# Performance work log

Hardware: AMD Instinct MI355X
Metric: run time of the kernel (lower is better)

Reference implementation:

```python
import jax, jax.numpy as jnp
import numpy as np

B, F, V, E = 16384, 20, 100000, 32
D_BOT = F * E            # 640
DIMS = (512, 256)        # bottom MLP dims
TDIMS = (128, 64)        # tower hidden dims
N_DOM = 4


def setup_inputs() -> dict:
    key = jax.random.key(0)
    ks = jax.random.split(key, 16)
    inp = {
        "feature_ids": jax.random.randint(ks[0], (B, F), 0, V, dtype=jnp.int64),
        "domain_id": jax.random.randint(ks[1], (B,), 0, N_DOM, dtype=jnp.int64),
        # embedding tables [F, V, E]
        "emb": jax.random.normal(ks[2], (F, V, E), dtype=jnp.float32) * 0.01,
        # bottom MLP: 640 -> 512 -> 256 (relu, no output layer)
        "W1": jax.random.normal(ks[3], (D_BOT, DIMS[0]), dtype=jnp.float32) * (1.0 / np.sqrt(D_BOT)),
        "b1": jnp.zeros((DIMS[0],), dtype=jnp.float32),
        "W2": jax.random.normal(ks[4], (DIMS[0], DIMS[1]), dtype=jnp.float32) * (1.0 / np.sqrt(DIMS[0])),
        "b2": jnp.zeros((DIMS[1],), dtype=jnp.float32),
        # towers (stacked over domain dim): 256 -> 128 -> 64 -> 1
        "TW1": jax.random.normal(ks[5], (N_DOM, DIMS[1], TDIMS[0]), dtype=jnp.float32) * (1.0 / np.sqrt(DIMS[1])),
        "Tb1": jnp.zeros((N_DOM, TDIMS[0]), dtype=jnp.float32),
        "TW2": jax.random.normal(ks[6], (N_DOM, TDIMS[0], TDIMS[1]), dtype=jnp.float32) * (1.0 / np.sqrt(TDIMS[0])),
        "Tb2": jnp.zeros((N_DOM, TDIMS[1]), dtype=jnp.float32),
        "TW3": jax.random.normal(ks[7], (N_DOM, TDIMS[1], 1), dtype=jnp.float32) * (1.0 / np.sqrt(TDIMS[1])),
        "Tb3": jnp.zeros((N_DOM, 1), dtype=jnp.float32),
    }
    return inp


def reference(feature_ids, domain_id, emb, W1, b1, W2, b2, TW1, Tb1, TW2, Tb2, TW3, Tb3):
    # Embedding lookup + concat: [B, F, E] -> [B, F*E]
    e = emb[jnp.arange(F)[None, :], feature_ids]          # [B, F, E]
    h = e.reshape(B, F * E)
    # Shared bottom MLP (relu)
    h = jax.nn.relu(h @ W1 + b1)                          # [B, 512]
    h = jax.nn.relu(h @ W2 + b2)                          # [B, 256]
    # All domain towers computed densely for every sample (faithful to source)
    t = jax.nn.relu(jnp.einsum('bi,dio->bdo', h, TW1) + Tb1[None])   # [B, D, 128]
    t = jax.nn.relu(jnp.einsum('bdi,dio->bdo', t, TW2) + Tb2[None])  # [B, D, 64]
    logit = jnp.einsum('bdi,dio->bdo', t, TW3) + Tb3[None]           # [B, D, 1]
    ys = jax.nn.sigmoid(logit)[..., 0]                    # [B, D]
    # Select per-sample domain output via mask (domains are exclusive)
    onehot = jax.nn.one_hot(domain_id, N_DOM, dtype=ys.dtype)        # [B, D]
    final = jnp.sum(ys * onehot, axis=1)                  # [B]
    return final
```

## Files before the change

### kernel.cpp

```cpp
#include <hip/hip_runtime.h>

#define B_SZ  16384
#define F_SZ  20
#define V_SZ  100000
#define E_SZ  32
#define DBOT  640
#define D1    512
#define D2    256
#define T1D   128
#define T2D   64
#define NDOM  4

typedef __bf16 bf16x8 __attribute__((ext_vector_type(8)));
typedef float  f32x4  __attribute__((ext_vector_type(4)));

#define MFMA(a, b, c) __builtin_amdgcn_mfma_f32_16x16x32_bf16((a), (b), (c), 0, 0, 0)

__global__ __launch_bounds__(256) void k_prep(const float* __restrict__ W1,
                                              const float* __restrict__ W2,
                                              const float* __restrict__ TW1,
                                              const float* __restrict__ TW2,
                                              __bf16* __restrict__ W1P,
                                              __bf16* __restrict__ W2P,
                                              __bf16* __restrict__ TW1P,
                                              __bf16* __restrict__ TW2P,
                                              int* __restrict__ cnt) {
  int bid = blockIdx.x, tid = threadIdx.x;
  const float* src; __bf16* dst; int n, k, N;
  if (bid < 160) {
    long g = (long)bid * 256 + tid;
    int lane = g & 63; int kkg = (int)((g >> 6) % 20); int ntile = (int)(g / 1280);
    n = ntile * 16 + (lane & 15); k = kkg * 32 + ((lane >> 4) << 3);
    src = W1; N = D1; dst = W1P + g * 8;
  } else if (bid < 224) {
    long g = (long)(bid - 160) * 256 + tid;
    int lane = g & 63; int kkg = (int)((g >> 6) & 15); int ntile = (int)(g >> 10);
    n = ntile * 16 + (lane & 15); k = kkg * 32 + ((lane >> 4) << 3);
    src = W2; N = D2; dst = W2P + g * 8;
  } else if (bid < 288) {
    long g = (long)(bid - 224) * 256 + tid;
    int d = (int)(g >> 12); long r = g & 4095;
    int lane = r & 63; int kkg = (int)((r >> 6) & 7); int ntile = (int)(r >> 9);
    n = ntile * 16 + (lane & 15); k = kkg * 32 + ((lane >> 4) << 3);
    src = TW1 + (long)d * D2 * T1D; N = T1D;
    dst = TW1P + ((long)(d * 64 + ntile * 8 + kkg) * 64 + lane) * 8;
  } else if (bid < 304) {
    long g = (long)(bid - 288) * 256 + tid;
    int d = (int)(g >> 10); long r = g & 1023;
    int lane = r & 63; int kkg = (int)((r >> 6) & 3); int ntile = (int)(r >> 8);
    n = ntile * 16 + (lane & 15); k = kkg * 32 + ((lane >> 4) << 3);
    src = TW2 + (long)d * T1D * T2D; N = T2D;
    dst = TW2P + ((long)(d * 16 + ntile * 4 + kkg) * 64 + lane) * 8;
  } else {
    if (tid < NDOM) cnt[tid] = 0;
    return;
  }
  bf16x8 o;
#pragma unroll
  for (int e = 0; e < 8; ++e) o[e] = (__bf16)src[(long)(k + e) * N + n];
  *(bf16x8*)dst = o;
}

__global__ __launch_bounds__(512) void k_fused(const int* __restrict__ fids,
                                               const int* __restrict__ dom,
                                               const float* __restrict__ emb,
                                               const __bf16* __restrict__ W1P,
                                               const float* __restrict__ b1,
                                               const __bf16* __restrict__ W2P,
                                               const float* __restrict__ b2,
                                               __bf16* __restrict__ h2,
                                               int* __restrict__ cnt,
                                               int* __restrict__ lists) {
  __shared__ int    ids_lds[64 * F_SZ];
  __shared__ __bf16 sA[64 * DBOT];
  __shared__ __bf16 h1[64 * D1];

  int bid = blockIdx.x, tid = threadIdx.x;
  int lane = tid & 63, w = tid >> 6;
  int lrow = lane & 15, kq = lane >> 4;
  int m0 = bid * 64;

  if (bid < 64 && tid < 256) {
    int i = bid * 256 + tid;
    int d = dom[i];
    int pl = tid & 63;
#pragma unroll
    for (int dd = 0; dd < NDOM; ++dd) {
      unsigned long long md = __ballot(d == dd);
      if (d == dd) {
        int myoff = __popcll(md & ((1ull << pl) - 1ull));
        int leader = __ffsll((long long)md) - 1;
        int base = 0;
        if (pl == leader) base = atomicAdd(&cnt[dd], __popcll(md));
        base = __shfl(base, leader);
        lists[dd * B_SZ + base + myoff] = i;
      }
    }
  }

  for (int i = tid; i < 64 * F_SZ; i += 512) ids_lds[i] = fids[m0 * F_SZ + i];
  __syncthreads();

  float4 ga[10], gb[10];
  int sb[10];
  {
#pragma unroll
    for (int i = 0; i < 10; ++i) {
      unsigned c = tid + i * 512;
      unsigned row = c / 80;
      unsigned cc = c - row * 80;
      int f = cc >> 2, es = (cc & 3) << 3;
      int id = ids_lds[row * F_SZ + f];
      const float* p = emb + ((long)f * V_SZ + id) * E_SZ + es;
      ga[i] = *(const float4*)p;
      gb[i] = *(const float4*)(p + 4);
      sb[i] = (int)(row * 1280 + cc * 16) ^ ((row & 7) << 4);
    }
#pragma unroll
    for (int i = 0; i < 10; ++i) {
      bf16x8 o;
      o[0] = (__bf16)ga[i].x; o[1] = (__bf16)ga[i].y;
      o[2] = (__bf16)ga[i].z; o[3] = (__bf16)ga[i].w;
      o[4] = (__bf16)gb[i].x; o[5] = (__bf16)gb[i].y;
      o[6] = (__bf16)gb[i].z; o[7] = (__bf16)gb[i].w;
      *(bf16x8*)((char*)sA + sb[i]) = o;
    }
  }
  __syncthreads();

  f32x4 acc[4][4] = {};
#pragma unroll
  for (int f = 0; f < F_SZ; ++f) {
    bf16x8 af[4];
#pragma unroll
    for (int mi = 0; mi < 4; ++mi) {
      int byte = ((mi * 16 + lrow) * 1280 + (f * 32 + kq * 8) * 2) ^ ((lrow & 7) << 4);
      af[mi] = *(const bf16x8*)((const char*)sA + byte);
    }
#pragma unroll
    for (int ni = 0; ni < 4; ++ni) {
      bf16x8 bfr = *(const bf16x8*)(W1P +
          ((long)((w * 4 + ni) * 20 + f) * 64 + lane) * 8);
#pragma unroll
      for (int mi = 0; mi < 4; ++mi)
        acc[mi][ni] = MFMA(af[mi], bfr, acc[mi][ni]);
    }
  }

#pragma unroll
  for (int ni = 0; ni < 4; ++ni) {
    int col = w * 64 + ni * 16 + lrow;
    float bv = b1[col];
#pragma unroll
    for (int mi = 0; mi < 4; ++mi) {
#pragma unroll
      for (int r = 0; r < 4; ++r) {
        int row = mi * 16 + kq * 4 + r;
        float v = acc[mi][ni][r] + bv;
        v = v > 0.f ? v : 0.f;
        int byte = (row * 1024 + col * 2) ^ ((row & 7) << 4);
        *(__bf16*)((char*)h1 + byte) = (__bf16)v;
      }
    }
  }
  __syncthreads();

  f32x4 acc2[4][2] = {};
#pragma unroll 4
  for (int kkg = 0; kkg < 16; ++kkg) {
    bf16x8 a2[4];
#pragma unroll
    for (int mi = 0; mi < 4; ++mi) {
      int byte = ((mi * 16 + lrow) * 1024 + kkg * 64 + kq * 16) ^ ((lrow & 7) << 4);
      a2[mi] = *(const bf16x8*)((const char*)h1 + byte);
    }
#pragma unroll
    for (int ni = 0; ni < 2; ++ni) {
      bf16x8 bfr = *(const bf16x8*)(W2P +
          ((long)((w * 2 + ni) * 16 + kkg) * 64 + lane) * 8);
#pragma unroll
      for (int mi = 0; mi < 4; ++mi)
        acc2[mi][ni] = MFMA(a2[mi], bfr, acc2[mi][ni]);
    }
  }

#pragma unroll
  for (int ni = 0; ni < 2; ++ni) {
    int col = w * 32 + ni * 16 + lrow;
    float bv = b2[col];
#pragma unroll
    for (int mi = 0; mi < 4; ++mi) {
#pragma unroll
      for (int r = 0; r < 4; ++r) {
        long row = m0 + mi * 16 + kq * 4 + r;
        float v = acc2[mi][ni][r] + bv;
        v = v > 0.f ? v : 0.f;
        h2[row * D2 + col] = (__bf16)v;
      }
    }
  }
}

__global__ __launch_bounds__(256) void k_tower(const __bf16* __restrict__ h2,
                                               const __bf16* __restrict__ TW1P,
                                               const __bf16* __restrict__ TW2P,
                                               const float* __restrict__ Tb1,
                                               const float* __restrict__ Tb2,
                                               const float* __restrict__ TW3,
                                               const float* __restrict__ Tb3,
                                               const int* __restrict__ cnt,
                                               const int* __restrict__ lists,
                                               float* __restrict__ out) {
  __shared__ __bf16 t_lds[4][16 * 128];
  int d  = blockIdx.y;
  int nc = cnt[d];
  int base = blockIdx.x * 64;
  if (base >= nc) return;

  int tid  = threadIdx.x;
  int lane = tid & 63;
  int w    = tid >> 6;
  int row  = lane & 15;
  int kq   = lane >> 4;
  int slot = base + w * 16 + row;
  bool valid = slot < nc;
  int m0r = lists[d * B_SZ + (valid ? slot : 0)];

  bf16x8 a1[8];
#pragma unroll
  for (int kk = 0; kk < 8; ++kk)
    a1[kk] = *(const bf16x8*)(h2 + (long)m0r * D2 + kk * 32 + kq * 8);

  f32x4 acc1[8] = {};
#pragma unroll
  for (int kk = 0; kk < 8; ++kk) {
#pragma unroll
    for (int ni = 0; ni < 8; ++ni) {
      bf16x8 b = *(const bf16x8*)(TW1P +
          ((long)(d * 64 + ni * 8 + kk) * 64 + lane) * 8);
      acc1[ni] = MFMA(a1[kk], b, acc1[ni]);
    }
  }
#pragma unroll
  for (int ni = 0; ni < 8; ++ni) {
    float bv = Tb1[d * T1D + ni * 16 + row];
#pragma unroll
    for (int r = 0; r < 4; ++r) {
      float v = acc1[ni][r] + bv;
      v = v > 0.f ? v : 0.f;
      t_lds[w][(kq * 4 + r) * 128 + ni * 16 + row] = (__bf16)v;
    }
  }
  asm volatile("s_waitcnt lgkmcnt(0)" ::: "memory");

  bf16x8 a2[4];
#pragma unroll
  for (int kk = 0; kk < 4; ++kk)
    a2[kk] = *(const bf16x8*)(&t_lds[w][row * 128 + kk * 32 + kq * 8]);
  f32x4 acc2[4] = {};
#pragma unroll
  for (int kk = 0; kk < 4; ++kk) {
#pragma unroll
    for (int ni = 0; ni < 4; ++ni) {
      bf16x8 b = *(const bf16x8*)(TW2P +
          ((long)(d * 16 + ni * 4 + kk) * 64 + lane) * 8);
      acc2[ni] = MFMA(a2[kk], b, acc2[ni]);
    }
  }
  asm volatile("s_waitcnt lgkmcnt(0)" ::: "memory");
#pragma unroll
  for (int ni = 0; ni < 4; ++ni) {
    float bv = Tb2[d * T2D + ni * 16 + row];
#pragma unroll
    for (int r = 0; r < 4; ++r) {
      float v = acc2[ni][r] + bv;
      v = v > 0.f ? v : 0.f;
      t_lds[w][(kq * 4 + r) * 64 + ni * 16 + row] = (__bf16)v;
    }
  }
  asm volatile("s_waitcnt lgkmcnt(0)" ::: "memory");

  float s = 0.f;
#pragma unroll
  for (int j = 0; j < 16; ++j)
    s += (float)t_lds[w][row * 64 + kq * 16 + j] * TW3[d * T2D + kq * 16 + j];
  s += __shfl_xor(s, 16);
  s += __shfl_xor(s, 32);
  s += Tb3[d];
  if (valid && kq == 0)
    out[m0r] = 1.0f / (1.0f + expf(-s));
}

extern "C" void kernel_launch(void* const* d_in, const int* in_sizes, int n_in,
                              void* d_out, int out_size, void* d_ws, size_t ws_size,
                              hipStream_t stream) {
  const int*   fids = (const int*)d_in[0];
  const int*   dom  = (const int*)d_in[1];
  const float* emb  = (const float*)d_in[2];
  const float* W1   = (const float*)d_in[3];
  const float* b1   = (const float*)d_in[4];
  const float* W2   = (const float*)d_in[5];
  const float* b2   = (const float*)d_in[6];
  const float* TW1  = (const float*)d_in[7];
  const float* Tb1  = (const float*)d_in[8];
  const float* TW2  = (const float*)d_in[9];
  const float* Tb2  = (const float*)d_in[10];
  const float* TW3  = (const float*)d_in[11];
  const float* Tb3  = (const float*)d_in[12];
  float* out = (float*)d_out;

  char* ws = (char*)d_ws;
  __bf16* W1P   = (__bf16*)(ws);
  __bf16* W2P   = (__bf16*)(ws + 655360);
  __bf16* TW1P  = (__bf16*)(ws + 917504);
  __bf16* TW2P  = (__bf16*)(ws + 1179648);
  __bf16* h2    = (__bf16*)(ws + 1245184);
  int*    lists = (int*)(ws + 9633792);
  int*    cnt   = (int*)(ws + 9895936);

  k_prep<<<305, 256, 0, stream>>>(W1, W2, TW1, TW2, W1P, W2P, TW1P, TW2P, cnt);
  k_fused<<<256, 512, 0, stream>>>(fids, dom, emb, W1P, b1, W2P, b2, h2,
                                   cnt, lists);
  k_tower<<<dim3(80, NDOM), 256, 0, stream>>>(h2, TW1P, TW2P, Tb1, Tb2,
                                              TW3, Tb3, cnt, lists, out);
}
```

Baseline: 53.16 us.

## Fuse tower MLPs into bottom-MLP kernel, computing all domains densely per tile

Merges the tower stage into the bottom-MLP kernel so h2 stays in LDS rather than going through global memory, and drops the separate tower launch. The per-domain bucketing with atomics and lists is replaced by computing all four towers densely for each 64-row tile and writing only the matching domain's output. This removes a kernel launch, the global h2 round trip and the atomic compaction, at the cost of four times the tower FLOPs and a larger shared-memory footprint (about 149 KB) that limits occupancy.

Result: faster. 50.03 us (-5.9%).

```diff
diff --git a/kernel.cpp b/kernel.cpp
--- a/kernel.cpp
+++ b/kernel.cpp
@@ -23,8 +23,7 @@
                                               __bf16* __restrict__ W1P,
                                               __bf16* __restrict__ W2P,
                                               __bf16* __restrict__ TW1P,
-                                              __bf16* __restrict__ TW2P,
-                                              int* __restrict__ cnt) {
+                                              __bf16* __restrict__ TW2P) {
   int bid = blockIdx.x, tid = threadIdx.x;
   const float* src; __bf16* dst; int n, k, N;
   if (bid < 160) {
@@ -44,16 +43,13 @@
     n = ntile * 16 + (lane & 15); k = kkg * 32 + ((lane >> 4) << 3);
     src = TW1 + (long)d * D2 * T1D; N = T1D;
     dst = TW1P + ((long)(d * 64 + ntile * 8 + kkg) * 64 + lane) * 8;
-  } else if (bid < 304) {
+  } else {
     long g = (long)(bid - 288) * 256 + tid;
     int d = (int)(g >> 10); long r = g & 1023;
     int lane = r & 63; int kkg = (int)((r >> 6) & 3); int ntile = (int)(r >> 8);
     n = ntile * 16 + (lane & 15); k = kkg * 32 + ((lane >> 4) << 3);
     src = TW2 + (long)d * T1D * T2D; N = T2D;
     dst = TW2P + ((long)(d * 16 + ntile * 4 + kkg) * 64 + lane) * 8;
-  } else {
-    if (tid < NDOM) cnt[tid] = 0;
-    return;
   }
   bf16x8 o;
 #pragma unroll
@@ -61,49 +57,38 @@
   *(bf16x8*)dst = o;
 }
 
-__global__ __launch_bounds__(512) void k_fused(const int* __restrict__ fids,
-                                               const int* __restrict__ dom,
-                                               const float* __restrict__ emb,
-                                               const __bf16* __restrict__ W1P,
-                                               const float* __restrict__ b1,
-                                               const __bf16* __restrict__ W2P,
-                                               const float* __restrict__ b2,
-                                               __bf16* __restrict__ h2,
-                                               int* __restrict__ cnt,
-                                               int* __restrict__ lists) {
-  __shared__ int    ids_lds[64 * F_SZ];
-  __shared__ __bf16 sA[64 * DBOT];
-  __shared__ __bf16 h1[64 * D1];
+__global__ __launch_bounds__(512) void k_mega(const int* __restrict__ fids,
+                                              const int* __restrict__ dom,
+                                              const float* __restrict__ emb,
+                                              const __bf16* __restrict__ W1P,
+                                              const float* __restrict__ b1,
+                                              const __bf16* __restrict__ W2P,
+                                              const float* __restrict__ b2,
+                                              const __bf16* __restrict__ TW1P,
+                                              const __bf16* __restrict__ TW2P,
+                                              const float* __restrict__ Tb1,
+                                              const float* __restrict__ Tb2,
+                                              const float* __restrict__ TW3,
+                                              const float* __restrict__ Tb3,
+                                              float* __restrict__ out) {
+  __shared__ __attribute__((aligned(16))) char smem[152576];
+  int*    ids_lds = (int*)(smem + 147456);
+  __bf16* sA      = (__bf16*)smem;
+  __bf16* h1      = (__bf16*)(smem + 81920);
+  __bf16* h2_lds  = (__bf16*)smem;
+  __bf16* t_lds   = (__bf16*)(smem + 32768);
 
   int bid = blockIdx.x, tid = threadIdx.x;
   int lane = tid & 63, w = tid >> 6;
   int lrow = lane & 15, kq = lane >> 4;
   int m0 = bid * 64;
 
-  if (bid < 64 && tid < 256) {
-    int i = bid * 256 + tid;
-    int d = dom[i];
-    int pl = tid & 63;
-#pragma unroll
-    for (int dd = 0; dd < NDOM; ++dd) {
-      unsigned long long md = __ballot(d == dd);
-      if (d == dd) {
-        int myoff = __popcll(md & ((1ull << pl) - 1ull));
-        int leader = __ffsll((long long)md) - 1;
-        int base = 0;
-        if (pl == leader) base = atomicAdd(&cnt[dd], __popcll(md));
-        base = __shfl(base, leader);
-        lists[dd * B_SZ + base + myoff] = i;
-      }
-    }
-  }
-
   for (int i = tid; i < 64 * F_SZ; i += 512) ids_lds[i] = fids[m0 * F_SZ + i];
   __syncthreads();
 
-  float4 ga[10], gb[10];
-  int sb[10];
-  {
+  {
+    float4 ga[10], gb[10];
+    int sb[10];
 #pragma unroll
     for (int i = 0; i < 10; ++i) {
       unsigned c = tid + i * 512;
@@ -128,167 +113,160 @@
   }
   __syncthreads();
 
-  f32x4 acc[4][4] = {};
-#pragma unroll
-  for (int f = 0; f < F_SZ; ++f) {
-    bf16x8 af[4];
-#pragma unroll
-    for (int mi = 0; mi < 4; ++mi) {
-      int byte = ((mi * 16 + lrow) * 1280 + (f * 32 + kq * 8) * 2) ^ ((lrow & 7) << 4);
-      af[mi] = *(const bf16x8*)((const char*)sA + byte);
+  {
+    f32x4 acc[4][4] = {};
+#pragma unroll
+    for (int f = 0; f < F_SZ; ++f) {
+      bf16x8 af[4];
+#pragma unroll
+      for (int mi = 0; mi < 4; ++mi) {
+        int byte = ((mi * 16 + lrow) * 1280 + (f * 32 + kq * 8) * 2) ^ ((lrow & 7) << 4);
+        af[mi] = *(const bf16x8*)((const char*)sA + byte);
+      }
+#pragma unroll
+      for (int ni = 0; ni < 4; ++ni) {
+        bf16x8 bfr = *(const bf16x8*)(W1P +
+            ((long)((w * 4 + ni) * 20 + f) * 64 + lane) * 8);
+#pragma unroll
+        for (int mi = 0; mi < 4; ++mi)
+          acc[mi][ni] = MFMA(af[mi], bfr, acc[mi][ni]);
+      }
     }
 #pragma unroll
     for (int ni = 0; ni < 4; ++ni) {
-      bf16x8 bfr = *(const bf16x8*)(W1P +
-          ((long)((w * 4 + ni) * 20 + f) * 64 + lane) * 8);
-#pragma unroll
-      for (int mi = 0; mi < 4; ++mi)
-        acc[mi][ni] = MFMA(af[mi], bfr, acc[mi][ni]);
-    }
-  }
-
-#pragma unroll
-  for (int ni = 0; ni < 4; ++ni) {
-    int col = w * 64 + ni * 16 + lrow;
-    float bv = b1[col];
-#pragma unroll
-    for (int mi = 0; mi < 4; ++mi) {
-#pragma unroll
-      for (int r = 0; r < 4; ++r) {
-        int row = mi * 16 + kq * 4 + r;
-        float v = acc[mi][ni][r] + bv;
-        v = v > 0.f ? v : 0.f;
-        int byte = (row * 1024 + col * 2) ^ ((row & 7) << 4);
-        *(__bf16*)((char*)h1 + byte) = (__bf16)v;
-      }
-    }
-  }
-  __syncthreads();
-
-  f32x4 acc2[4][2] = {};
+      int col = w * 64 + ni * 16 + lrow;
+      float bv = b1[col];
+#pragma unroll
+      for (int mi = 0; mi < 4; ++mi) {
+#pragma unroll
+        for (int r = 0; r < 4; ++r) {
+          int row = mi * 16 + kq * 4 + r;
+          float v = acc[mi][ni][r] + bv;
+          v = v > 0.f ? v : 0.f;
+          int byte = (row * 1024 + col * 2) ^ ((row & 7) << 4);
+          *(__bf16*)((char*)h1 + byte) = (__bf16)v;
+        }
+      }
+    }
+  }
+  __syncthreads();
+
+  {
+    f32x4 acc2[4][2] = {};
 #pragma unroll 4
-  for (int kkg = 0; kkg < 16; ++kkg) {
-    bf16x8 a2[4];
-#pragma unroll
-    for (int mi = 0; mi < 4; ++mi) {
-      int byte = ((mi * 16 + lrow) * 1024 + kkg * 64 + kq * 16) ^ ((lrow & 7) << 4);
-      a2[mi] = *(const bf16x8*)((const char*)h1 + byte);
+    for (int kkg = 0; kkg < 16; ++kkg) {
+      bf16x8 a2[4];
+#pragma unroll
+      for (int mi = 0; mi < 4; ++mi) {
+        int byte = ((mi * 16 + lrow) * 1024 + kkg * 64 + kq * 16) ^ ((lrow & 7) << 4);
+        a2[mi] = *(const bf16x8*)((const char*)h1 + byte);
+      }
+#pragma unroll
+      for (int ni = 0; ni < 2; ++ni) {
+        bf16x8 bfr = *(const bf16x8*)(W2P +
+            ((long)((w * 2 + ni) * 16 + kkg) * 64 + lane) * 8);
+#pragma unroll
+        for (int mi = 0; mi < 4; ++mi)
+          acc2[mi][ni] = MFMA(a2[mi], bfr, acc2[mi][ni]);
+      }
     }
 #pragma unroll
     for (int ni = 0; ni < 2; ++ni) {
-      bf16x8 bfr = *(const bf16x8*)(W2P +
-          ((long)((w * 2 + ni) * 16 + kkg) * 64 + lane) * 8);
-#pragma unroll
-      for (int mi = 0; mi < 4; ++mi)
-        acc2[mi][ni] = MFMA(a2[mi], bfr, acc2[mi][ni]);
-    }
-  }
-
-#pragma unroll
-  for (int ni = 0; ni < 2; ++ni) {
-    int col = w * 32 + ni * 16 + lrow;
-    float bv = b2[col];
-#pragma unroll
-    for (int mi = 0; mi < 4; ++mi) {
-#pragma unroll
-      for (int r = 0; r < 4; ++r) {
-        long row = m0 + mi * 16 + kq * 4 + r;
-        float v = acc2[mi][ni][r] + bv;
-        v = v > 0.f ? v : 0.f;
-        h2[row * D2 + col] = (__bf16)v;
-      }
-    }
-  }
-}
-
-__global__ __launch_bounds__(256) void k_tower(const __bf16* __restrict__ h2,
-                                               const __bf16* __restrict__ TW1P,
-                                               const __bf16* __restrict__ TW2P,
-                                               const float* __restrict__ Tb1,
-                                               const float* __restrict__ Tb2,
-                                               const float* __restrict__ TW3,
-                                               const float* __restrict__ Tb3,
-                                               const int* __restrict__ cnt,
-                                               const int* __restrict__ lists,
-                                               float* __restrict__ out) {
-  __shared__ __bf16 t_lds[4][16 * 128];
-  int d  = blockIdx.y;
-  int nc = cnt[d];
-  int base = blockIdx.x * 64;
-  if (base >= nc) return;
-
-  int tid  = threadIdx.x;
-  int lane = tid & 63;
-  int w    = tid >> 6;
-  int row  = lane & 15;
-  int kq   = lane >> 4;
-  int slot = base + w * 16 + row;
-  bool valid = slot < nc;
-  int m0r = lists[d * B_SZ + (valid ? slot : 0)];
-
-  bf16x8 a1[8];
-#pragma unroll
-  for (int kk = 0; kk < 8; ++kk)
-    a1[kk] = *(const bf16x8*)(h2 + (long)m0r * D2 + kk * 32 + kq * 8);
-
-  f32x4 acc1[8] = {};
-#pragma unroll
-  for (int kk = 0; kk < 8; ++kk) {
-#pragma unroll
-    for (int ni = 0; ni < 8; ++ni) {
-      bf16x8 b = *(const bf16x8*)(TW1P +
-          ((long)(d * 64 + ni * 8 + kk) * 64 + lane) * 8);
-      acc1[ni] = MFMA(a1[kk], b, acc1[ni]);
-    }
-  }
-#pragma unroll
-  for (int ni = 0; ni < 8; ++ni) {
-    float bv = Tb1[d * T1D + ni * 16 + row];
-#pragma unroll
-    for (int r = 0; r < 4; ++r) {
-      float v = acc1[ni][r] + bv;
-      v = v > 0.f ? v : 0.f;
-      t_lds[w][(kq * 4 + r) * 128 + ni * 16 + row] = (__bf16)v;
-    }
-  }
-  asm volatile("s_waitcnt lgkmcnt(0)" ::: "memory");
-
-  bf16x8 a2[4];
-#pragma unroll
-  for (int kk = 0; kk < 4; ++kk)
-    a2[kk] = *(const bf16x8*)(&t_lds[w][row * 128 + kk * 32 + kq * 8]);
-  f32x4 acc2[4] = {};
-#pragma unroll
-  for (int kk = 0; kk < 4; ++kk) {
-#pragma unroll
-    for (int ni = 0; ni < 4; ++ni) {
-      bf16x8 b = *(const bf16x8*)(TW2P +
-          ((long)(d * 16 + ni * 4 + kk) * 64 + lane) * 8);
-      acc2[ni] = MFMA(a2[kk], b, acc2[ni]);
-    }
-  }
-  asm volatile("s_waitcnt lgkmcnt(0)" ::: "memory");
-#pragma unroll
-  for (int ni = 0; ni < 4; ++ni) {
-    float bv = Tb2[d * T2D + ni * 16 + row];
-#pragma unroll
-    for (int r = 0; r < 4; ++r) {
-      float v = acc2[ni][r] + bv;
-      v = v > 0.f ? v : 0.f;
-      t_lds[w][(kq * 4 + r) * 64 + ni * 16 + row] = (__bf16)v;
-    }
-  }
-  asm volatile("s_waitcnt lgkmcnt(0)" ::: "memory");
-
-  float s = 0.f;
-#pragma unroll
-  for (int j = 0; j < 16; ++j)
-    s += (float)t_lds[w][row * 64 + kq * 16 + j] * TW3[d * T2D + kq * 16 + j];
-  s += __shfl_xor(s, 16);
-  s += __shfl_xor(s, 32);
-  s += Tb3[d];
-  if (valid && kq == 0)
-    out[m0r] = 1.0f / (1.0f + expf(-s));
+      int col = w * 32 + ni * 16 + lrow;
+      float bv = b2[col];
+#pragma unroll
+      for (int mi = 0; mi < 4; ++mi) {
+#pragma unroll
+        for (int r = 0; r < 4; ++r) {
+          int row = mi * 16 + kq * 4 + r;
+          float v = acc2[mi][ni][r] + bv;
+          v = v > 0.f ? v : 0.f;
+          int byte = (row * 512 + col * 2) ^ ((row & 7) << 4);
+          *(__bf16*)((char*)h2_lds + byte) = (__bf16)v;
+        }
+      }
+    }
+  }
+  __syncthreads();
+
+  {
+    int r0 = (w & 3) * 16;
+    int d0 = (w >> 2) * 2;
+    int grow = r0 + lrow;
+    int mydom = dom[m0 + grow];
+    __bf16* tw = t_lds + w * 2048;
+
+    bf16x8 a1[8];
+#pragma unroll
+    for (int kk = 0; kk < 8; ++kk) {
+      int byte = (grow * 512 + (kk * 32 + kq * 8) * 2) ^ ((grow & 7) << 4);
+      a1[kk] = *(const bf16x8*)((const char*)h2_lds + byte);
+    }
+
+#pragma unroll
+    for (int dd = 0; dd < 2; ++dd) {
+      int d = d0 + dd;
+      f32x4 acc1[8] = {};
+#pragma unroll
+      for (int kk = 0; kk < 8; ++kk) {
+#pragma unroll
+        for (int ni = 0; ni < 8; ++ni) {
+          bf16x8 b = *(const bf16x8*)(TW1P +
+              ((long)(d * 64 + ni * 8 + kk) * 64 + lane) * 8);
+          acc1[ni] = MFMA(a1[kk], b, acc1[ni]);
+        }
+      }
+#pragma unroll
+      for (int ni = 0; ni < 8; ++ni) {
+        float bv = Tb1[d * T1D + ni * 16 + lrow];
+#pragma unroll
+        for (int r = 0; r < 4; ++r) {
+          float v = acc1[ni][r] + bv;
+          v = v > 0.f ? v : 0.f;
+          tw[(kq * 4 + r) * 128 + ni * 16 + lrow] = (__bf16)v;
+        }
+      }
+      asm volatile("s_waitcnt lgkmcnt(0)" ::: "memory");
+
+      bf16x8 a2f[4];
+#pragma unroll
+      for (int kk = 0; kk < 4; ++kk)
+        a2f[kk] = *(const bf16x8*)(&tw[lrow * 128 + kk * 32 + kq * 8]);
+      f32x4 acc2[4] = {};
+#pragma unroll
+      for (int kk = 0; kk < 4; ++kk) {
+#pragma unroll
+        for (int ni = 0; ni < 4; ++ni) {
+          bf16x8 b = *(const bf16x8*)(TW2P +
+              ((long)(d * 16 + ni * 4 + kk) * 64 + lane) * 8);
+          acc2[ni] = MFMA(a2f[kk], b, acc2[ni]);
+        }
+      }
+      asm volatile("s_waitcnt lgkmcnt(0)" ::: "memory");
+#pragma unroll
+      for (int ni = 0; ni < 4; ++ni) {
+        float bv = Tb2[d * T2D + ni * 16 + lrow];
+#pragma unroll
+        for (int r = 0; r < 4; ++r) {
+          float v = acc2[ni][r] + bv;
+          v = v > 0.f ? v : 0.f;
+          tw[(kq * 4 + r) * 64 + ni * 16 + lrow] = (__bf16)v;
+        }
+      }
+      asm volatile("s_waitcnt lgkmcnt(0)" ::: "memory");
+
+      float s = 0.f;
+#pragma unroll
+      for (int j = 0; j < 16; ++j)
+        s += (float)tw[lrow * 64 + kq * 16 + j] * TW3[d * T2D + kq * 16 + j];
+      s += __shfl_xor(s, 16);
+      s += __shfl_xor(s, 32);
+      s += Tb3[d];
+      if (kq == 0 && mydom == d)
+        out[m0 + grow] = 1.0f / (1.0f + expf(-s));
+      asm volatile("s_waitcnt lgkmcnt(0)" ::: "memory");
+    }
+  }
 }
 
 extern "C" void kernel_launch(void* const* d_in, const int* in_sizes, int n_in,
@@ -314,13 +292,8 @@
   __bf16* W2P   = (__bf16*)(ws + 655360);
   __bf16* TW1P  = (__bf16*)(ws + 917504);
   __bf16* TW2P  = (__bf16*)(ws + 1179648);
-  __bf16* h2    = (__bf16*)(ws + 1245184);
-  int*    lists = (int*)(ws + 9633792);
-  int*    cnt   = (int*)(ws + 9895936);
-
-  k_prep<<<305, 256, 0, stream>>>(W1, W2, TW1, TW2, W1P, W2P, TW1P, TW2P, cnt);
-  k_fused<<<256, 512, 0, stream>>>(fids, dom, emb, W1P, b1, W2P, b2, h2,
-                                   cnt, lists);
-  k_tower<<<dim3(80, NDOM), 256, 0, stream>>>(h2, TW1P, TW2P, Tb1, Tb2,
-                                              TW3, Tb3, cnt, lists, out);
+
+  k_prep<<<304, 256, 0, stream>>>(W1, W2, TW1, TW2, W1P, W2P, TW1P, TW2P);
+  k_mega<<<256, 512, 0, stream>>>(fids, dom, emb, W1P, b1, W2P, b2,
+                                  TW1P, TW2P, Tb1, Tb2, TW3, Tb3, out);
 }
```
